# Kernel tuning notes

Hardware: AMD Instinct MI355X
Metric: run time of the kernel (lower is better)

The kernel has to match this reference:

```python
import jax, jax.numpy as jnp
import numpy as np

B, NU, NX, NW, NY, T = 64, 64, 128, 128, 32, 2048


def setup_inputs() -> dict:
    key = jax.random.key(0)
    ks = jax.random.split(key, 14)
    u = jax.random.normal(ks[0], (B, NU, T), dtype=jnp.float32)
    # E initialized at identity in the module; add small perturbation so inverse is nontrivial
    E = jnp.eye(NX, dtype=jnp.float32) + 0.01 * jax.random.normal(ks[1], (NX, NX), dtype=jnp.float32)
    # Recurrent matrices scaled for stability over 2048 steps
    F_w = 0.3 * jax.random.normal(ks[2], (NX, NX), dtype=jnp.float32) / np.sqrt(NX)
    F_b = jnp.zeros((NX,), dtype=jnp.float32)
    B1_w = 0.3 * jax.random.normal(ks[3], (NX, NW), dtype=jnp.float32) / np.sqrt(NW)
    B2_w = 0.3 * jax.random.normal(ks[4], (NX, NU), dtype=jnp.float32) / np.sqrt(NU)
    C2tild = jax.random.normal(ks[5], (NW, NX), dtype=jnp.float32) / np.sqrt(NX)
    Dtild = jax.random.normal(ks[6], (NW, NU), dtype=jnp.float32) / np.sqrt(NU)
    bv = jax.random.uniform(ks[7], (NW,), dtype=jnp.float32) - 0.5
    # IQC multipliers: positive (Neuron method is a per-neuron diagonal)
    lam = 0.5 + jax.random.uniform(ks[8], (NW,), dtype=jnp.float32)
    C1_w = jax.random.normal(ks[9], (NY, NX), dtype=jnp.float32) / np.sqrt(NX)
    D11_w = jax.random.normal(ks[10], (NY, NW), dtype=jnp.float32) / np.sqrt(NW)
    D12_w = jax.random.normal(ks[11], (NY, NU), dtype=jnp.float32) / np.sqrt(NU)
    by = jnp.zeros((NY,), dtype=jnp.float32)
    return {"u": u, "E": E, "F_w": F_w, "F_b": F_b, "B1_w": B1_w, "B2_w": B2_w,
            "C2tild": C2tild, "Dtild": Dtild, "bv": bv, "lam": lam,
            "C1_w": C1_w, "D11_w": D11_w, "D12_w": D12_w, "by": by}


def reference(u, E, F_w, F_b, B1_w, B2_w, C2tild, Dtild, bv, lam, C1_w, D11_w, D12_w, by):
    inputs = jnp.transpose(u, (0, 2, 1))          # (b, T, nu)
    b, seq_len, _ = inputs.shape
    nx = F_w.shape[0]
    Einv = jnp.linalg.inv(E)
    inv_lam = 1.0 / lam
    Cv = inv_lam[:, None] * C2tild                 # diag(1/lam) @ C2tild, (nw, nx)
    Dv = inv_lam[:, None] * Dtild                  # (nw, nu)

    h0 = jnp.zeros((b, nx), dtype=inputs.dtype)

    def step(ht, ut):
        vt = ht @ Cv.T + ut @ Dv.T + bv            # (b, nw)
        wt = jax.nn.relu(vt)
        eh = ht @ F_w.T + F_b + wt @ B1_w.T + ut @ B2_w.T
        ht1 = eh @ Einv.T
        return ht1, ht1

    us = jnp.swapaxes(inputs[:, :-1, :], 0, 1)     # (T-1, b, nu)
    _, states_rest = jax.lax.scan(step, h0, us)    # (T-1, b, nx)
    states = jnp.concatenate([h0[None], states_rest], axis=0)  # (T, b, nx)
    states = jnp.swapaxes(states, 0, 1)            # (b, T, nx)

    W = jax.nn.relu(states @ Cv.T + inputs @ Dv.T + bv)        # (b, T, nw)
    yest = states @ C1_w.T + W @ D11_w.T + inputs @ D12_w.T + by  # (b, T, ny)
    return jnp.transpose(yest, (0, 2, 1))          # (b, ny, T)
```

## Files before the change

kernel.cpp:

```cpp
#include <hip/hip_runtime.h>

#define TD 2048

#define OFF_X0    0
#define OFF_X1    16384
#define OFF_TB    32768
#define OFF_W1T   49152
#define OFF_W2T   81920
#define OFF_WGH   98304
#define OFF_BIAS  114688
#define OFF_C1T   114944
#define OFF_D11T  119040
#define OFF_D12T  123136
#define OFF_BY    125184
#define OFF_HST   125216
#define OFF_GHY   135168

__device__ __forceinline__ float quad_sum(float x) {
  int v = __builtin_bit_cast(int, x);
  v = __builtin_amdgcn_update_dpp(0, v, 0xB1, 0xF, 0xF, true);
  x += __builtin_bit_cast(float, v);
  v = __builtin_bit_cast(int, x);
  v = __builtin_amdgcn_update_dpp(0, v, 0x4E, 0xF, 0xF, true);
  x += __builtin_bit_cast(float, v);
  return x;
}

__device__ __forceinline__ void wg_barrier_lds() {
  asm volatile("s_waitcnt lgkmcnt(0)" ::: "memory");
  __builtin_amdgcn_s_barrier();
  __builtin_amdgcn_sched_barrier(0);
}

__global__ void k_prep(const float* __restrict__ E, const float* __restrict__ C2,
                       const float* __restrict__ Dt, const float* __restrict__ D12,
                       const float* __restrict__ bv, const float* __restrict__ by,
                       const float* __restrict__ C1w, const float* __restrict__ D11w,
                       const float* __restrict__ lam, float* __restrict__ ws)
{
  const int n = 59552;
  for (int e = blockIdx.x * blockDim.x + threadIdx.x; e < n; e += gridDim.x * blockDim.x) {
    int x = e;
    if (x < 16384) { int i = x >> 7, j = x & 127;
      ws[OFF_X0 + x] = (i == j ? 2.f : 0.f) - E[x]; continue; }
    x -= 16384;
    if (x < 16384) { int k = x >> 7, r = x & 127;
      ws[OFF_W1T + k * 256 + r] = C2[r * 128 + k] / lam[r]; continue; }
    x -= 16384;
    if (x < 8192) { int k = x >> 7, j = x & 127;
      ws[OFF_WGH + k * 256 + j] = Dt[j * 64 + k] / lam[j]; continue; }
    x -= 8192;
    if (x < 2048) { int k = x >> 5, r = x & 31;
      ws[OFF_D12T + k * 32 + r] = D12[r * 64 + k]; continue; }
    x -= 2048;
    if (x < 128) { ws[OFF_BIAS + x] = bv[x]; continue; }
    x -= 128;
    if (x < 32) { ws[OFF_BY + x] = by[x]; continue; }
    x -= 32;
    if (x < 4096) { int i = x >> 5, r = x & 31;
      ws[OFF_C1T + i * 32 + r] = C1w[r * 128 + i]; continue; }
    x -= 4096;
    if (x < 4096) { int i = x >> 5, r = x & 31;
      ws[OFF_D11T + i * 32 + r] = D11w[r * 128 + i]; continue; }
    x -= 4096;
    ws[OFF_HST + x] = 0.f;
  }
}

__global__ void k_mm1(const float* __restrict__ E, const float* __restrict__ X,
                      float* __restrict__ Tb)
{
  __shared__ float er[128];
  const int i = blockIdx.x, j = threadIdx.x;
  er[j] = E[i * 128 + j];
  __syncthreads();
  float acc = 0.f;
#pragma unroll 8
  for (int m = 0; m < 128; ++m) acc = fmaf(er[m], X[m * 128 + j], acc);
  Tb[i * 128 + j] = acc;
}

__global__ void k_mm2(const float* __restrict__ X, const float* __restrict__ Tb,
                      float* __restrict__ Xn)
{
  __shared__ float xr[128];
  const int i = blockIdx.x, j = threadIdx.x;
  xr[j] = X[i * 128 + j];
  __syncthreads();
  float acc = 0.f;
#pragma unroll 8
  for (int m = 0; m < 128; ++m) acc = fmaf(xr[m], Tb[m * 128 + j], acc);
  Xn[i * 128 + j] = 2.f * X[i * 128 + j] - acc;
}

__global__ void k_fold(const float* __restrict__ Einv, const float* __restrict__ Fw,
                       const float* __restrict__ B1w, const float* __restrict__ B2w,
                       const float* __restrict__ Fb, float* __restrict__ ws)
{
  __shared__ float ei[128];
  const int i = blockIdx.x, tid = threadIdx.x;
  if (tid < 128) ei[tid] = Einv[i * 128 + tid];
  __syncthreads();
  if (tid < 128) {
    float fh = 0.f, bh1 = 0.f;
#pragma unroll 4
    for (int m = 0; m < 128; ++m) {
      fh  = fmaf(ei[m], Fw[m * 128 + tid], fh);
      bh1 = fmaf(ei[m], B1w[m * 128 + tid], bh1);
    }
    ws[OFF_W1T + tid * 256 + 128 + i] = fh;
    ws[OFF_W2T + tid * 128 + i] = bh1;
  } else if (tid < 192) {
    const int k = tid - 128;
    float bh2 = 0.f;
#pragma unroll 4
    for (int m = 0; m < 128; ++m) bh2 = fmaf(ei[m], B2w[m * 64 + k], bh2);
    ws[OFF_WGH + k * 256 + 128 + i] = bh2;
  } else if (tid == 192) {
    float fb = 0.f;
    for (int m = 0; m < 128; ++m) fb = fmaf(ei[m], Fb[m], fb);
    ws[OFF_BIAS + 128 + i] = fb;
  }
}

__global__ __launch_bounds__(256, 1) void k_pre(
    const float* __restrict__ u, const float* __restrict__ WGH,
    const float* __restrict__ bias, float* __restrict__ GHY, int t_base, int Tc)
{
  const int b = blockIdx.y;
  const int tc0 = blockIdx.x * 32;
  const int tid = threadIdx.x;
  __shared__ __align__(16) float wl[64 * 256];
  for (int c = tid; c < 64 * 256 / 4; c += 256)
    *(float4*)&wl[c * 4] = *(const float4*)&WGH[c * 4];
  __syncthreads();
  float acc[32];
  const float bj = bias[tid];
#pragma unroll
  for (int i = 0; i < 32; ++i) acc[i] = bj;
  const float* ub = u + ((size_t)b * 64) * TD + t_base + tc0;
  for (int k = 0; k < 64; ++k) {
    const float* uk = ub + (size_t)k * TD;
    const float w = wl[k * 256 + tid];
#pragma unroll
    for (int c4 = 0; c4 < 8; ++c4) {
      const float4 uv = *(const float4*)&uk[c4 * 4];
      acc[c4 * 4 + 0] = fmaf(w, uv.x, acc[c4 * 4 + 0]);
      acc[c4 * 4 + 1] = fmaf(w, uv.y, acc[c4 * 4 + 1]);
      acc[c4 * 4 + 2] = fmaf(w, uv.z, acc[c4 * 4 + 2]);
      acc[c4 * 4 + 3] = fmaf(w, uv.w, acc[c4 * 4 + 3]);
    }
  }
  float* gout = GHY + ((size_t)b * Tc + tc0) * 256 + tid;
#pragma unroll
  for (int i = 0; i < 32; ++i) gout[(size_t)i * 256] = acc[i];
}

__global__ __launch_bounds__(512, 2) void k_serial(
    const float* __restrict__ W1t, const float* __restrict__ W2t,
    float* __restrict__ GHY, float* __restrict__ hbT, float* __restrict__ hstate,
    int t_base, int Tc)
{
  const int b = blockIdx.x;
  const int tid = threadIdx.x;
  const int lane = tid & 63;
  const int wave = tid >> 6;
  const int q = lane & 3;
  const int rp = lane >> 2;
  const int r0 = wave * 32 + rp * 2;
  const int row2 = wave * 16 + rp;
  const int hq = q * 36;

  __shared__ __align__(16) float hbufs[2][144];
  __shared__ __align__(16) float wl[144];
  __shared__ __align__(16) float pf[128];

  float w1a[32], w1b[32], w2[32];
#pragma unroll
  for (int kk = 0; kk < 32; ++kk) {
    const float2 wv = *(const float2*)&W1t[(q * 32 + kk) * 256 + r0];
    w1a[kk] = wv.x; w1b[kk] = wv.y;
    w2[kk] = W2t[(q * 32 + kk) * 128 + row2];
  }

  if (tid < 128) {
    const float hv0 = hstate[(size_t)b * 128 + tid];
    hbufs[0][(tid >> 5) * 36 + (tid & 31)] = hv0;
    hbT[((size_t)b * 128 + tid) * Tc] = hv0;
  }

  const size_t ghbase = (size_t)b * Tc * 256;
  float2 ghc = *(const float2*)&GHY[ghbase + r0];
  __syncthreads();

  float* hc = hbufs[0];
  float* hn = hbufs[1];

  for (int tc = 0; tc < Tc; ++tc) {
    const int tn = (tc + 1 < Tc) ? (tc + 1) : tc;
    const float2 ghn = *(const float2*)&GHY[ghbase + (size_t)tn * 256 + r0];

    float a0 = 0.f, a1 = 0.f;
#pragma unroll
    for (int k8 = 0; k8 < 8; ++k8) {
      const float4 hv = *(const float4*)&hc[hq + k8 * 4];
      a0 = fmaf(w1a[k8 * 4 + 0], hv.x, a0); a1 = fmaf(w1b[k8 * 4 + 0], hv.x, a1);
      a0 = fmaf(w1a[k8 * 4 + 1], hv.y, a0); a1 = fmaf(w1b[k8 * 4 + 1], hv.y, a1);
      a0 = fmaf(w1a[k8 * 4 + 2], hv.z, a0); a1 = fmaf(w1b[k8 * 4 + 2], hv.z, a1);
      a0 = fmaf(w1a[k8 * 4 + 3], hv.w, a0); a1 = fmaf(w1b[k8 * 4 + 3], hv.w, a1);
    }
    a0 = quad_sum(a0); a1 = quad_sum(a1);
    float x0 = a0 + ghc.x, x1 = a1 + ghc.y;
    if (wave < 4) {
      x0 = fmaxf(x0, 0.f); x1 = fmaxf(x1, 0.f);
      if (q == 0) {
        *(float2*)&wl[(r0 >> 5) * 36 + (r0 & 31)] = make_float2(x0, x1);
        *(float2*)&GHY[ghbase + (size_t)tc * 256 + r0] = make_float2(x0, x1);
      }
    } else {
      if (q == 0) *(float2*)&pf[r0 - 128] = make_float2(x0, x1);
    }
    wg_barrier_lds();
    if (t_base + tc == TD - 1) break;

    float a2 = 0.f;
#pragma unroll
    for (int k8 = 0; k8 < 8; ++k8) {
      const float4 wv = *(const float4*)&wl[hq + k8 * 4];
      a2 = fmaf(w2[k8 * 4 + 0], wv.x, a2);
      a2 = fmaf(w2[k8 * 4 + 1], wv.y, a2);
      a2 = fmaf(w2[k8 * 4 + 2], wv.z, a2);
      a2 = fmaf(w2[k8 * 4 + 3], wv.w, a2);
    }
    a2 = quad_sum(a2);
    if (q == 0) {
      const float hp = a2 + pf[row2];
      hn[(row2 >> 5) * 36 + (row2 & 31)] = hp;
      if (tc + 1 < Tc) hbT[((size_t)b * 128 + row2) * Tc + (tc + 1)] = hp;
      else             hstate[(size_t)b * 128 + row2] = hp;
    }
    wg_barrier_lds();
    float* tmp = hc; hc = hn; hn = tmp;
    ghc = ghn;
  }
}

__global__ __launch_bounds__(256, 2) void k_post(
    const float* __restrict__ hbT, const float* __restrict__ GHY,
    const float* __restrict__ C1T, const float* __restrict__ D11T,
    const float* __restrict__ D12T, const float* __restrict__ BY,
    const float* __restrict__ u, float* __restrict__ y, int t_base, int Tc)
{
  const int b = blockIdx.y;
  const int tc0 = blockIdx.x * 32;
  const int tid = threadIdx.x;
  __shared__ __align__(16) float hT[128 * 36];
  __shared__ __align__(16) float wT[128 * 36];
  __shared__ __align__(16) float uT[64 * 36];
  {
    const int i = tid >> 1, half = tid & 1;
    const float* hsrc = hbT + ((size_t)b * 128 + i) * Tc + tc0 + half * 16;
    float* hdst = &hT[i * 36 + half * 16];
#pragma unroll
    for (int c = 0; c < 4; ++c) *(float4*)&hdst[c * 4] = *(const float4*)&hsrc[c * 4];
    const float* wsrc = GHY + ((size_t)b * Tc + tc0 + half * 16) * 256 + i;
    float* wdst = &wT[i * 36 + half * 16];
#pragma unroll
    for (int tt = 0; tt < 16; ++tt) wdst[tt] = wsrc[(size_t)tt * 256];
    if (tid < 128) {
      const float* usrc = u + ((size_t)b * 64 + i) * TD + t_base + tc0 + half * 16;
      float* udst = &uT[i * 36 + half * 16];
#pragma unroll
      for (int c = 0; c < 4; ++c) *(float4*)&udst[c * 4] = *(const float4*)&usrc[c * 4];
    }
  }
  __syncthreads();
  const int jp = tid >> 4;
  const int tq = tid & 15;
  float a00 = 0.f, a01 = 0.f, a10 = 0.f, a11 = 0.f;
#pragma unroll 4
  for (int i = 0; i < 128; ++i) {
    const float2 cv = *(const float2*)&C1T[i * 32 + 2 * jp];
    const float2 hv = *(const float2*)&hT[i * 36 + 2 * tq];
    const float2 dv = *(const float2*)&D11T[i * 32 + 2 * jp];
    const float2 wv = *(const float2*)&wT[i * 36 + 2 * tq];
    a00 = fmaf(cv.x, hv.x, a00); a00 = fmaf(dv.x, wv.x, a00);
    a01 = fmaf(cv.x, hv.y, a01); a01 = fmaf(dv.x, wv.y, a01);
    a10 = fmaf(cv.y, hv.x, a10); a10 = fmaf(dv.y, wv.x, a10);
    a11 = fmaf(cv.y, hv.y, a11); a11 = fmaf(dv.y, wv.y, a11);
  }
#pragma unroll 4
  for (int k = 0; k < 64; ++k) {
    const float2 ev = *(const float2*)&D12T[k * 32 + 2 * jp];
    const float2 uv = *(const float2*)&uT[k * 36 + 2 * tq];
    a00 = fmaf(ev.x, uv.x, a00); a01 = fmaf(ev.x, uv.y, a01);
    a10 = fmaf(ev.y, uv.x, a10); a11 = fmaf(ev.y, uv.y, a11);
  }
  const int j0 = 2 * jp;
  const int tA = t_base + tc0 + 2 * tq;
  const float by0 = BY[j0], by1 = BY[j0 + 1];
  float* yo = y + ((size_t)b * 32 + j0) * TD + tA;
  *(float2*)yo = make_float2(a00 + by0, a01 + by0);
  *(float2*)(yo + TD) = make_float2(a10 + by1, a11 + by1);
}

__global__ void k_sentinel(float* out, float mb) {
  if (threadIdx.x == 0 && blockIdx.x == 0) out[0] = -1.0e6f - mb;
}

extern "C" void kernel_launch(void* const* d_in, const int* in_sizes, int n_in,
                              void* d_out, int out_size, void* d_ws, size_t ws_size,
                              hipStream_t stream)
{
  (void)in_sizes; (void)n_in;
  const float* u    = (const float*)d_in[0];
  const float* E    = (const float*)d_in[1];
  const float* Fw   = (const float*)d_in[2];
  const float* Fb   = (const float*)d_in[3];
  const float* B1w  = (const float*)d_in[4];
  const float* B2w  = (const float*)d_in[5];
  const float* C2   = (const float*)d_in[6];
  const float* Dt   = (const float*)d_in[7];
  const float* bv   = (const float*)d_in[8];
  const float* lam  = (const float*)d_in[9];
  const float* C1w  = (const float*)d_in[10];
  const float* D11w = (const float*)d_in[11];
  const float* D12w = (const float*)d_in[12];
  const float* by   = (const float*)d_in[13];
  float* ws = (float*)d_ws;
  float* y = (float*)d_out;

  const size_t avail = ws_size / 4;
  int Tc = TD;
  while (Tc >= 64) {
    const unsigned long long need = OFF_GHY + 24576ull * (unsigned)Tc;
    if (need <= (unsigned long long)avail) break;
    Tc >>= 1;
  }
  if (Tc < 64) {
    hipMemsetAsync(d_out, 0, (size_t)out_size * 4, stream);
    k_sentinel<<<dim3(1), dim3(64), 0, stream>>>(y, (float)(ws_size >> 20));
    return;
  }
  float* GHY = ws + OFF_GHY;
  float* HBT = GHY + 16384ull * (unsigned)Tc;

  k_prep<<<dim3(64), dim3(256), 0, stream>>>(E, C2, Dt, D12w, bv, by, C1w, D11w, lam, ws);

  float* cur = ws + OFF_X0;
  float* nxt = ws + OFF_X1;
  float* Tb = ws + OFF_TB;
  for (int it = 0; it < 4; ++it) {
    k_mm1<<<dim3(128), dim3(128), 0, stream>>>(E, cur, Tb);
    k_mm2<<<dim3(128), dim3(128), 0, stream>>>(cur, Tb, nxt);
    float* t2 = cur; cur = nxt; nxt = t2;
  }
  k_fold<<<dim3(128), dim3(256), 0, stream>>>(cur, Fw, B1w, B2w, Fb, ws);

  for (int t0 = 0; t0 < TD; t0 += Tc) {
    k_pre<<<dim3(Tc / 32, 64), dim3(256), 0, stream>>>(u, ws + OFF_WGH, ws + OFF_BIAS,
                                                       GHY, t0, Tc);
    k_serial<<<dim3(64), dim3(512), 0, stream>>>(ws + OFF_W1T, ws + OFF_W2T,
                                                 GHY, HBT, ws + OFF_HST, t0, Tc);
    k_post<<<dim3(Tc / 32, 64), dim3(256), 0, stream>>>(HBT, GHY, ws + OFF_C1T,
                                                        ws + OFF_D11T, ws + OFF_D12T,
                                                        ws + OFF_BY, u, y, t0, Tc);
  }
}
```

Before: 1.818 ms.

## Fold B1 into recurrence state to make serial loop one fused matvec per step

```diff
diff --git a/kernel.cpp b/kernel.cpp
--- a/kernel.cpp
+++ b/kernel.cpp
@@ -5,16 +5,18 @@
 #define OFF_X0    0
 #define OFF_X1    16384
 #define OFF_TB    32768
-#define OFF_W1T   49152
-#define OFF_W2T   81920
-#define OFF_WGH   98304
-#define OFF_BIAS  114688
-#define OFF_C1T   114944
-#define OFF_D11T  119040
-#define OFF_D12T  123136
-#define OFF_BY    125184
-#define OFF_HST   125216
-#define OFF_GHY   135168
+#define OFF_MT    49152
+#define OFF_W2T   114688
+#define OFF_WGH   131072
+#define OFF_BIAS  147456
+#define OFF_C1T   147712
+#define OFF_C1B   151808
+#define OFF_D11T  155904
+#define OFF_D12T  160000
+#define OFF_BY    162048
+#define OFF_PST   162080
+#define OFF_WST   178464
+#define OFF_GHY   194880
 
 __device__ __forceinline__ float quad_sum(float x) {
   int v = __builtin_bit_cast(int, x);
@@ -38,14 +40,14 @@
                        const float* __restrict__ C1w, const float* __restrict__ D11w,
                        const float* __restrict__ lam, float* __restrict__ ws)
 {
-  const int n = 59552;
+  const int n = 67744;
   for (int e = blockIdx.x * blockDim.x + threadIdx.x; e < n; e += gridDim.x * blockDim.x) {
     int x = e;
     if (x < 16384) { int i = x >> 7, j = x & 127;
       ws[OFF_X0 + x] = (i == j ? 2.f : 0.f) - E[x]; continue; }
     x -= 16384;
     if (x < 16384) { int k = x >> 7, r = x & 127;
-      ws[OFF_W1T + k * 256 + r] = C2[r * 128 + k] / lam[r]; continue; }
+      ws[OFF_MT + k * 256 + r] = C2[r * 128 + k] / lam[r]; continue; }
     x -= 16384;
     if (x < 8192) { int k = x >> 7, j = x & 127;
       ws[OFF_WGH + k * 256 + j] = Dt[j * 64 + k] / lam[j]; continue; }
@@ -63,7 +65,9 @@
     if (x < 4096) { int i = x >> 5, r = x & 31;
       ws[OFF_D11T + i * 32 + r] = D11w[r * 128 + i]; continue; }
     x -= 4096;
-    ws[OFF_HST + x] = 0.f;
+    if (x < 8192) { ws[OFF_PST + x] = 0.f; continue; }
+    x -= 8192;
+    ws[OFF_WST + x] = 0.f;
   }
 }
 
@@ -108,7 +112,7 @@
       fh  = fmaf(ei[m], Fw[m * 128 + tid], fh);
       bh1 = fmaf(ei[m], B1w[m * 128 + tid], bh1);
     }
-    ws[OFF_W1T + tid * 256 + 128 + i] = fh;
+    ws[OFF_MT + tid * 256 + 128 + i] = fh;
     ws[OFF_W2T + tid * 128 + i] = bh1;
   } else if (tid < 192) {
     const int k = tid - 128;
@@ -123,6 +127,27 @@
   }
 }
 
+__global__ __launch_bounds__(256, 4) void k_fold2(float* __restrict__ ws)
+{
+  const int kw = blockIdx.x;
+  const int tid = threadIdx.x;
+  __shared__ float bcol[128];
+  if (tid < 128) bcol[tid] = ws[OFF_W2T + kw * 128 + tid];
+  __syncthreads();
+  float acc = 0.f;
+#pragma unroll 4
+  for (int m = 0; m < 128; ++m)
+    acc = fmaf(ws[OFF_MT + m * 256 + tid], bcol[m], acc);
+  ws[OFF_MT + (128 + kw) * 256 + tid] = acc;
+  if (tid < 32) {
+    float c1b = 0.f;
+#pragma unroll 4
+    for (int m = 0; m < 128; ++m)
+      c1b = fmaf(ws[OFF_C1T + m * 32 + tid], bcol[m], c1b);
+    ws[OFF_C1B + kw * 32 + tid] = c1b;
+  }
+}
+
 __global__ __launch_bounds__(256, 1) void k_pre(
     const float* __restrict__ u, const float* __restrict__ WGH,
     const float* __restrict__ bias, float* __restrict__ GHY, int t_base, int Tc)
@@ -156,117 +181,114 @@
   for (int i = 0; i < 32; ++i) gout[(size_t)i * 256] = acc[i];
 }
 
-__global__ __launch_bounds__(512, 2) void k_serial(
-    const float* __restrict__ W1t, const float* __restrict__ W2t,
-    float* __restrict__ GHY, float* __restrict__ hbT, float* __restrict__ hstate,
-    int t_base, int Tc)
+__global__ __launch_bounds__(1024, 1) void k_serial(
+    const float* __restrict__ MT, float* __restrict__ GHY, float* __restrict__ pbT,
+    const float* __restrict__ pst_in, float* __restrict__ pst_out,
+    const float* __restrict__ wst_in, float* __restrict__ wst_out, int Tc)
 {
   const int b = blockIdx.x;
   const int tid = threadIdx.x;
-  const int lane = tid & 63;
-  const int wave = tid >> 6;
-  const int q = lane & 3;
-  const int rp = lane >> 2;
-  const int r0 = wave * 32 + rp * 2;
-  const int row2 = wave * 16 + rp;
-  const int hq = q * 36;
-
-  __shared__ __align__(16) float hbufs[2][144];
-  __shared__ __align__(16) float wl[144];
-  __shared__ __align__(16) float pf[128];
-
-  float w1a[32], w1b[32], w2[32];
-#pragma unroll
-  for (int kk = 0; kk < 32; ++kk) {
-    const float2 wv = *(const float2*)&W1t[(q * 32 + kk) * 256 + r0];
-    w1a[kk] = wv.x; w1b[kk] = wv.y;
-    w2[kk] = W2t[(q * 32 + kk) * 128 + row2];
-  }
+  const int q = tid & 3;
+  const int r = tid >> 2;
+  const int kb = q * 64;
+  const int wq = q * 68;
+
+  __shared__ __align__(16) float S[2][272];
+
+  float wgt[64];
+#pragma unroll
+  for (int kk = 0; kk < 64; ++kk) wgt[kk] = MT[(kb + kk) * 256 + r];
+
+  const bool isv = (r < 128);
+  const int pr = isv ? 0 : (r - 128);
 
   if (tid < 128) {
-    const float hv0 = hstate[(size_t)b * 128 + tid];
-    hbufs[0][(tid >> 5) * 36 + (tid & 31)] = hv0;
-    hbT[((size_t)b * 128 + tid) * Tc] = hv0;
-  }
-
-  const size_t ghbase = (size_t)b * Tc * 256;
-  float2 ghc = *(const float2*)&GHY[ghbase + r0];
-  __syncthreads();
-
-  float* hc = hbufs[0];
-  float* hn = hbufs[1];
-
-  for (int tc = 0; tc < Tc; ++tc) {
-    const int tn = (tc + 1 < Tc) ? (tc + 1) : tc;
-    const float2 ghn = *(const float2*)&GHY[ghbase + (size_t)tn * 256 + r0];
-
-    float a0 = 0.f, a1 = 0.f;
-#pragma unroll
-    for (int k8 = 0; k8 < 8; ++k8) {
-      const float4 hv = *(const float4*)&hc[hq + k8 * 4];
-      a0 = fmaf(w1a[k8 * 4 + 0], hv.x, a0); a1 = fmaf(w1b[k8 * 4 + 0], hv.x, a1);
-      a0 = fmaf(w1a[k8 * 4 + 1], hv.y, a0); a1 = fmaf(w1b[k8 * 4 + 1], hv.y, a1);
-      a0 = fmaf(w1a[k8 * 4 + 2], hv.z, a0); a1 = fmaf(w1b[k8 * 4 + 2], hv.z, a1);
-      a0 = fmaf(w1a[k8 * 4 + 3], hv.w, a0); a1 = fmaf(w1b[k8 * 4 + 3], hv.w, a1);
-    }
-    a0 = quad_sum(a0); a1 = quad_sum(a1);
-    float x0 = a0 + ghc.x, x1 = a1 + ghc.y;
-    if (wave < 4) {
-      x0 = fmaxf(x0, 0.f); x1 = fmaxf(x1, 0.f);
-      if (q == 0) {
-        *(float2*)&wl[(r0 >> 5) * 36 + (r0 & 31)] = make_float2(x0, x1);
-        *(float2*)&GHY[ghbase + (size_t)tc * 256 + r0] = make_float2(x0, x1);
+    const float pv = pst_in[b * 128 + tid];
+    S[0][(tid >> 6) * 68 + (tid & 63)] = pv;
+    pbT[((size_t)b * 128 + tid) * Tc] = pv;
+  } else if (tid < 256) {
+    const int wi = tid - 128;
+    S[0][((128 + wi) >> 6) * 68 + ((128 + wi) & 63)] = wst_in[b * 128 + wi];
+  }
+
+  const float* gp = GHY + (size_t)b * Tc * 256 + r;
+  float* gw = GHY + (size_t)b * Tc * 256 + r;
+  float* pb = pbT + ((size_t)b * 128 + pr) * Tc + 1;
+  float gcur = gp[0];
+  __syncthreads();
+
+  int cur = 0;
+  for (int t = 0; t < Tc; ++t) {
+    const float gn = gp[256];
+    gp += 256;
+    const float* Sc = S[cur];
+    float acc0 = 0.f, acc1 = 0.f, acc2 = 0.f, acc3 = 0.f;
+#pragma unroll
+    for (int c = 0; c < 4; ++c) {
+      float hv[16];
+      *(float4*)&hv[0]  = *(const float4*)&Sc[wq + c * 16 + 0];
+      *(float4*)&hv[4]  = *(const float4*)&Sc[wq + c * 16 + 4];
+      *(float4*)&hv[8]  = *(const float4*)&Sc[wq + c * 16 + 8];
+      *(float4*)&hv[12] = *(const float4*)&Sc[wq + c * 16 + 12];
+#pragma unroll
+      for (int j = 0; j < 4; ++j) {
+        acc0 = fmaf(wgt[c * 16 + j * 4 + 0], hv[j * 4 + 0], acc0);
+        acc1 = fmaf(wgt[c * 16 + j * 4 + 1], hv[j * 4 + 1], acc1);
+        acc2 = fmaf(wgt[c * 16 + j * 4 + 2], hv[j * 4 + 2], acc2);
+        acc3 = fmaf(wgt[c * 16 + j * 4 + 3], hv[j * 4 + 3], acc3);
       }
-    } else {
-      if (q == 0) *(float2*)&pf[r0 - 128] = make_float2(x0, x1);
-    }
+    }
+    float a = (acc0 + acc1) + (acc2 + acc3);
+    a = quad_sum(a);
+    float* Sn = S[cur ^ 1];
+    if (q == 0) {
+      float x = a + gcur;
+      if (isv) {
+        x = fmaxf(x, 0.f);
+        Sn[((128 + r) >> 6) * 68 + ((128 + r) & 63)] = x;
+        gw[0] = x;
+        if (t == Tc - 1) wst_out[b * 128 + r] = x;
+      } else {
+        Sn[(pr >> 6) * 68 + (pr & 63)] = x;
+        if (t + 1 < Tc) pb[t] = x;
+        else            pst_out[b * 128 + pr] = x;
+      }
+    }
+    gw += 256;
     wg_barrier_lds();
-    if (t_base + tc == TD - 1) break;
-
-    float a2 = 0.f;
-#pragma unroll
-    for (int k8 = 0; k8 < 8; ++k8) {
-      const float4 wv = *(const float4*)&wl[hq + k8 * 4];
-      a2 = fmaf(w2[k8 * 4 + 0], wv.x, a2);
-      a2 = fmaf(w2[k8 * 4 + 1], wv.y, a2);
-      a2 = fmaf(w2[k8 * 4 + 2], wv.z, a2);
-      a2 = fmaf(w2[k8 * 4 + 3], wv.w, a2);
-    }
-    a2 = quad_sum(a2);
-    if (q == 0) {
-      const float hp = a2 + pf[row2];
-      hn[(row2 >> 5) * 36 + (row2 & 31)] = hp;
-      if (tc + 1 < Tc) hbT[((size_t)b * 128 + row2) * Tc + (tc + 1)] = hp;
-      else             hstate[(size_t)b * 128 + row2] = hp;
-    }
-    wg_barrier_lds();
-    float* tmp = hc; hc = hn; hn = tmp;
-    ghc = ghn;
+    cur ^= 1;
+    gcur = gn;
   }
 }
 
 __global__ __launch_bounds__(256, 2) void k_post(
-    const float* __restrict__ hbT, const float* __restrict__ GHY,
-    const float* __restrict__ C1T, const float* __restrict__ D11T,
-    const float* __restrict__ D12T, const float* __restrict__ BY,
-    const float* __restrict__ u, float* __restrict__ y, int t_base, int Tc)
+    const float* __restrict__ pbT, const float* __restrict__ GHY,
+    const float* __restrict__ C1T, const float* __restrict__ C1BT,
+    const float* __restrict__ D11T, const float* __restrict__ D12T,
+    const float* __restrict__ BY, const float* __restrict__ u,
+    const float* __restrict__ wprev, float* __restrict__ y, int t_base, int Tc)
 {
   const int b = blockIdx.y;
   const int tc0 = blockIdx.x * 32;
   const int tid = threadIdx.x;
-  __shared__ __align__(16) float hT[128 * 36];
-  __shared__ __align__(16) float wT[128 * 36];
+  __shared__ __align__(16) float pT[128 * 36];
+  __shared__ __align__(16) float wT[128 * 40];
   __shared__ __align__(16) float uT[64 * 36];
   {
     const int i = tid >> 1, half = tid & 1;
-    const float* hsrc = hbT + ((size_t)b * 128 + i) * Tc + tc0 + half * 16;
-    float* hdst = &hT[i * 36 + half * 16];
-#pragma unroll
-    for (int c = 0; c < 4; ++c) *(float4*)&hdst[c * 4] = *(const float4*)&hsrc[c * 4];
-    const float* wsrc = GHY + ((size_t)b * Tc + tc0 + half * 16) * 256 + i;
-    float* wdst = &wT[i * 36 + half * 16];
-#pragma unroll
-    for (int tt = 0; tt < 16; ++tt) wdst[tt] = wsrc[(size_t)tt * 256];
+    const float* psrc = pbT + ((size_t)b * 128 + i) * Tc + tc0 + half * 16;
+    float* pdst = &pT[i * 36 + half * 16];
+#pragma unroll
+    for (int c = 0; c < 4; ++c) *(float4*)&pdst[c * 4] = *(const float4*)&psrc[c * 4];
+    const float* gb = GHY + (size_t)b * Tc * 256;
+    if (half == 0) {
+      wT[i * 40] = (tc0 == 0) ? wprev[b * 128 + i] : gb[(size_t)(tc0 - 1) * 256 + i];
+#pragma unroll
+      for (int c = 1; c <= 16; ++c) wT[i * 40 + c] = gb[(size_t)(tc0 - 1 + c) * 256 + i];
+    } else {
+#pragma unroll
+      for (int c = 17; c <= 32; ++c) wT[i * 40 + c] = gb[(size_t)(tc0 - 1 + c) * 256 + i];
+    }
     if (tid < 128) {
       const float* usrc = u + ((size_t)b * 64 + i) * TD + t_base + tc0 + half * 16;
       float* udst = &uT[i * 36 + half * 16];
@@ -281,13 +303,16 @@
 #pragma unroll 4
   for (int i = 0; i < 128; ++i) {
     const float2 cv = *(const float2*)&C1T[i * 32 + 2 * jp];
-    const float2 hv = *(const float2*)&hT[i * 36 + 2 * tq];
+    const float2 pv = *(const float2*)&pT[i * 36 + 2 * tq];
+    const float2 cb = *(const float2*)&C1BT[i * 32 + 2 * jp];
     const float2 dv = *(const float2*)&D11T[i * 32 + 2 * jp];
-    const float2 wv = *(const float2*)&wT[i * 36 + 2 * tq];
-    a00 = fmaf(cv.x, hv.x, a00); a00 = fmaf(dv.x, wv.x, a00);
-    a01 = fmaf(cv.x, hv.y, a01); a01 = fmaf(dv.x, wv.y, a01);
-    a10 = fmaf(cv.y, hv.x, a10); a10 = fmaf(dv.y, wv.x, a10);
-    a11 = fmaf(cv.y, hv.y, a11); a11 = fmaf(dv.y, wv.y, a11);
+    const float w0 = wT[i * 40 + 2 * tq];
+    const float w1 = wT[i * 40 + 2 * tq + 1];
+    const float w2 = wT[i * 40 + 2 * tq + 2];
+    a00 = fmaf(cv.x, pv.x, a00); a00 = fmaf(cb.x, w0, a00); a00 = fmaf(dv.x, w1, a00);
+    a01 = fmaf(cv.x, pv.y, a01); a01 = fmaf(cb.x, w1, a01); a01 = fmaf(dv.x, w2, a01);
+    a10 = fmaf(cv.y, pv.x, a10); a10 = fmaf(cb.y, w0, a10); a10 = fmaf(dv.y, w1, a10);
+    a11 = fmaf(cv.y, pv.y, a11); a11 = fmaf(cb.y, w1, a11); a11 = fmaf(dv.y, w2, a11);
   }
 #pragma unroll 4
   for (int k = 0; k < 64; ++k) {
@@ -343,7 +368,7 @@
     return;
   }
   float* GHY = ws + OFF_GHY;
-  float* HBT = GHY + 16384ull * (unsigned)Tc;
+  float* PBT = GHY + 16384ull * (unsigned)Tc;
 
   k_prep<<<dim3(64), dim3(256), 0, stream>>>(E, C2, Dt, D12w, bv, by, C1w, D11w, lam, ws);
 
@@ -356,14 +381,21 @@
     float* t2 = cur; cur = nxt; nxt = t2;
   }
   k_fold<<<dim3(128), dim3(256), 0, stream>>>(cur, Fw, B1w, B2w, Fb, ws);
-
-  for (int t0 = 0; t0 < TD; t0 += Tc) {
+  k_fold2<<<dim3(128), dim3(256), 0, stream>>>(ws);
+
+  int c = 0;
+  for (int t0 = 0; t0 < TD; t0 += Tc, ++c) {
+    float* pin  = ws + OFF_PST + (size_t)(c & 1) * 8192;
+    float* pout = ws + OFF_PST + (size_t)((c + 1) & 1) * 8192;
+    float* win  = ws + OFF_WST + (size_t)(c & 1) * 8192;
+    float* wout = ws + OFF_WST + (size_t)((c + 1) & 1) * 8192;
     k_pre<<<dim3(Tc / 32, 64), dim3(256), 0, stream>>>(u, ws + OFF_WGH, ws + OFF_BIAS,
                                                        GHY, t0, Tc);
-    k_serial<<<dim3(64), dim3(512), 0, stream>>>(ws + OFF_W1T, ws + OFF_W2T,
-                                                 GHY, HBT, ws + OFF_HST, t0, Tc);
-    k_post<<<dim3(Tc / 32, 64), dim3(256), 0, stream>>>(HBT, GHY, ws + OFF_C1T,
-                                                        ws + OFF_D11T, ws + OFF_D12T,
-                                                        ws + OFF_BY, u, y, t0, Tc);
-  }
-}
+    k_serial<<<dim3(64), dim3(1024), 0, stream>>>(ws + OFF_MT, GHY, PBT,
+                                                  pin, pout, win, wout, Tc);
+    k_post<<<dim3(Tc / 32, 64), dim3(256), 0, stream>>>(PBT, GHY, ws + OFF_C1T,
+                                                        ws + OFF_C1B, ws + OFF_D11T,
+                                                        ws + OFF_D12T, ws + OFF_BY,
+                                                        u, win, y, t0, Tc);
+  }
+}
```

After: 1.752 ms. 1.04x faster.
